# Optimization experiments

Measured on AMD Instinct MI355X. Metric: run time of the kernel, lower is better.

The kernel has to match this reference:

```python
import jax, jax.numpy as jnp
import numpy as np

NEG_INF = jnp.float32(-1e30)
EPS = 1e-7  # keras.backend.ctc_batch_cost epsilon


def ctc_batch_cost(y_true, y_pred):
    """Faithful CTC loss (keras ctc_batch_cost semantics): y_pred are
    probabilities [B,T,C], blank = C-1, full input/label lengths.
    Returns per-example negative log likelihood [B,1]."""
    B, T, C = y_pred.shape
    L = y_true.shape[1]
    S = 2 * L + 1  # extended label length (blanks interleaved)
    blank = C - 1

    log_probs = jnp.log(y_pred + EPS)  # [B,T,C]

    # Extended label sequence: blank, l0, blank, l1, ..., blank  -> [B,S]
    ext = jnp.full((B, S), blank, dtype=y_true.dtype)
    ext = ext.at[:, 1::2].set(y_true)

    # Skip transition allowed at s if ext[s] != blank and ext[s] != ext[s-2]
    skip = jnp.concatenate(
        [jnp.zeros((B, 2), dtype=bool),
         (ext[:, 2:] != blank) & (ext[:, 2:] != ext[:, :-2])], axis=1)  # [B,S]

    # Gather log-probs of extended labels per timestep: [T,B,S]
    lp_ext = jnp.take_along_axis(log_probs, ext[:, None, :], axis=2)  # [B,T,S]
    lp_ext = jnp.transpose(lp_ext, (1, 0, 2))  # [T,B,S]

    # alpha init at t=0: only positions 0 (blank) and 1 (first label)
    alpha0 = jnp.full((B, S), NEG_INF, dtype=log_probs.dtype)
    alpha0 = alpha0.at[:, 0].set(lp_ext[0, :, 0])
    alpha0 = alpha0.at[:, 1].set(lp_ext[0, :, 1])

    pad1 = jnp.full((B, 1), NEG_INF, dtype=log_probs.dtype)
    pad2 = jnp.full((B, 2), NEG_INF, dtype=log_probs.dtype)

    def step(alpha, lp_t):
        a_stay = alpha
        a_prev = jnp.concatenate([pad1, alpha[:, :-1]], axis=1)
        a_skip = jnp.where(skip, jnp.concatenate([pad2, alpha[:, :-2]], axis=1), NEG_INF)
        m = jnp.maximum(jnp.maximum(a_stay, a_prev), a_skip)
        lse = m + jnp.log(jnp.exp(a_stay - m) + jnp.exp(a_prev - m) + jnp.exp(a_skip - m))
        return lse + lp_t, None

    alpha_T, _ = jax.lax.scan(step, alpha0, lp_ext[1:])  # [B,S]

    # log P = logsumexp over last blank and last label positions
    end = jnp.stack([alpha_T[:, S - 1], alpha_T[:, S - 2]], axis=1)  # [B,2]
    loglik = jax.nn.logsumexp(end, axis=1)  # [B]
    return -loglik[:, None]  # [B,1] like keras ctc_batch_cost


def setup_inputs() -> dict:
    key = jax.random.key(0)
    k1, k2 = jax.random.split(key)
    B, T, C, L = 512, 512, 128, 32
    y_true = jax.random.randint(k1, (B, L), 0, C - 1, dtype=jnp.int64 if jax.config.read('jax_enable_x64') else jnp.int32)
    y_pred = jax.random.uniform(k2, (B, T, C), dtype=jnp.float32)
    return {"y_true": y_true, "y_pred": y_pred}


def reference(y_true, y_pred):
    return ctc_batch_cost(y_true, y_pred)
```

## Files before the change

### kernel.cpp

```cpp
#include <hip/hip_runtime.h>


#define EPSF 1e-7f

constexpr int T_  = 512;
constexpr int C_  = 128;
constexpr int L_  = 32;
constexpr int NG  = 127;
constexpr int PFG = 4;
constexpr int NLD = 17;

__launch_bounds__(64)
__global__ void ctc_loss_kernel(const int* __restrict__ y_true,
                                const float* __restrict__ y_pred,
                                float* __restrict__ out) {
    const int b    = blockIdx.x;
    const int lane = threadIdx.x;

    const float* bb  = y_pred + (size_t)b * T_ * C_;
    const int*   lbl = y_true + b * L_;

    int   cls[7];
    float sg[7];
#pragma unroll
    for (int i = 0; i < 7; ++i) {
        const int v = lane - i;
        int   c = C_ - 1;
        float s = 0.f;
        if (v >= 1 && (v & 1)) {
            c = lbl[(v - 1) >> 1];
            if (v >= 3 && c != lbl[((v - 1) >> 1) - 1]) s = 1.f;
        }
        cls[i] = c;
        sg[i]  = s;
    }
    float msk[9];
#pragma unroll
    for (int i = 0; i < 9; ++i) msk[i] = (lane >= i) ? 1.f : 0.f;

    float a       = (lane < 2) ? (bb[cls[0]] + EPSF) : 0.f;
    float a64     = 0.f;
    int   e_total = 0;

    float Q[PFG][NLD];
    auto loadq = [&](float (&Qk)[NLD], const float* __restrict__ r) {
        Qk[0]  = r[cls[0]];          Qk[1]  = r[cls[1]];
        Qk[2]  = r[cls[2]];          Qk[3]  = r[cls[3]];
        Qk[4]  = r[cls[4]];          Qk[5]  = r[cls[5]];
        Qk[6]  = r[cls[6]];
        Qk[7]  = r[C_ + cls[0]];     Qk[8]  = r[C_ + cls[1]];
        Qk[9]  = r[C_ + cls[2]];     Qk[10] = r[C_ + cls[3]];
        Qk[11] = r[C_ + cls[4]];
        Qk[12] = r[2 * C_ + cls[0]]; Qk[13] = r[2 * C_ + cls[1]];
        Qk[14] = r[2 * C_ + cls[2]];
        Qk[15] = r[3 * C_ + cls[0]]; Qk[16] = r[3 * C_ + cls[1]];
    };
#pragma unroll
    for (int k = 0; k < PFG; ++k) loadq(Q[k], bb + (size_t)(1 + 4 * k) * C_);

    float smp[16];
    auto sample = [&]() {
#pragma unroll
        for (int i = 0; i < 16; ++i) smp[i] = __shfl(a, 4 * i + 3);
    };
    sample();

    auto group4 = [&](float (&Qk)[NLD]) {
        float A[9];
        A[0] = a;
#pragma unroll
        for (int i = 1; i <= 8; ++i) A[i] = __shfl_up(a, i) * msk[i];

        float B[7];
#pragma unroll
        for (int i = 0; i <= 6; ++i)
            B[i] = (A[i] + A[i + 1] + sg[i] * A[i + 2]) * (Qk[i] + EPSF);
        float Cc[5];
#pragma unroll
        for (int i = 0; i <= 4; ++i)
            Cc[i] = (B[i] + B[i + 1] + sg[i] * B[i + 2]) * (Qk[7 + i] + EPSF);
        float D[3];
#pragma unroll
        for (int i = 0; i <= 2; ++i)
            D[i] = (Cc[i] + Cc[i + 1] + sg[i] * Cc[i + 2]) * (Qk[12 + i] + EPSF);

        float z = a64;
        z = (z + A[0])  * (Qk[1]  + EPSF);
        z = (z + B[0])  * (Qk[8]  + EPSF);
        z = (z + Cc[0]) * (Qk[13] + EPSF);
        z = (z + D[0])  * (Qk[16] + EPSF);
        a64 = z;

        a = (D[0] + D[1] + sg[0] * D[2]) * (Qk[15] + EPSF);
    };

    auto apply_scale = [&]() {
        float t[8];
#pragma unroll
        for (int i = 0; i < 8; ++i) t[i] = fmaxf(smp[i], smp[i + 8]);
#pragma unroll
        for (int i = 0; i < 4; ++i) t[i] = fmaxf(t[i], t[i + 4]);
        float m = fmaxf(fmaxf(t[0], t[1]), fmaxf(t[2], t[3]));
        m = fmaxf(m, 1e-30f);
        const unsigned eb = __float_as_uint(m) >> 23;
        e_total += (int)eb - 127;
        const float inv = __uint_as_float((254u - eb) << 23);
        a *= inv;
        a64 *= inv;
    };

    for (int g0 = 0; g0 < 124; g0 += PFG) {
#pragma unroll
        for (int k = 0; k < PFG; ++k) {
            const int g = g0 + k;
            group4(Q[k]);
            apply_scale();
            sample();
            const int gn = g + PFG;
            if (gn < NG) loadq(Q[k], bb + (size_t)(1 + 4 * gn) * C_);
        }
    }

    float qo[3], qb[3];
#pragma unroll
    for (int r = 0; r < 3; ++r) {
        const float* rp = bb + (size_t)(509 + r) * C_;
        qo[r] = rp[cls[0]];
        qb[r] = rp[cls[1]];
    }

    group4(Q[0]); apply_scale(); sample();
    group4(Q[1]); apply_scale(); sample();
    group4(Q[2]); apply_scale();

#pragma unroll
    for (int r = 0; r < 3; ++r) {
        float prev = __shfl_up(a, 1) * msk[1];
        float sk   = __shfl_up(a, 2) * msk[2];
        const float anew = (a + prev + sg[0] * sk) * (qo[r] + EPSF);
        a64 = (a64 + a) * (qb[r] + EPSF);
        a = anew;
    }

    if (lane == 63) {
        out[b] = -(__logf(a + a64) + (float)e_total * 0.6931471805599453f);
    }
}

extern "C" void kernel_launch(void* const* d_in, const int* in_sizes, int n_in,
                              void* d_out, int out_size, void* d_ws, size_t ws_size,
                              hipStream_t stream) {
    const int*   y_true = (const int*)d_in[0];
    const float* y_pred = (const float*)d_in[1];
    float*       out    = (float*)d_out;

    const int B = out_size;
    ctc_loss_kernel<<<B, 64, 0, stream>>>(y_true, y_pred, out);
}
```

Measured before the change: 225.3 us.

## Split CTC recursion into concurrent forward and backward passes meeting mid-sequence

Result: no change. 226.5 us (+0.6%).

```diff
diff --git a/kernel.cpp b/kernel.cpp
--- a/kernel.cpp
+++ b/kernel.cpp
@@ -3,74 +3,103 @@
 
 #define EPSF 1e-7f
 
-constexpr int T_  = 512;
-constexpr int C_  = 128;
-constexpr int L_  = 32;
-constexpr int NG  = 127;
-constexpr int PFG = 4;
-constexpr int NLD = 17;
+constexpr int T_ = 512;
+constexpr int C_ = 128;
+constexpr int L_ = 32;
+constexpr int NF = 17;
+constexpr int NB = 28;
 
 __launch_bounds__(64)
 __global__ void ctc_loss_kernel(const int* __restrict__ y_true,
                                 const float* __restrict__ y_pred,
                                 float* __restrict__ out) {
-    const int b    = blockIdx.x;
+    const int bidx = blockIdx.x;
     const int lane = threadIdx.x;
 
-    const float* bb  = y_pred + (size_t)b * T_ * C_;
-    const int*   lbl = y_true + b * L_;
-
-    int   cls[7];
+    const float* bb  = y_pred + (size_t)bidx * T_ * C_;
+    const int*   lbl = y_true + bidx * L_;
+
+    int   cf[7];
     float sg[7];
+    float msk[9];
 #pragma unroll
     for (int i = 0; i < 7; ++i) {
         const int v = lane - i;
-        int   c = C_ - 1;
-        float s = 0.f;
+        int c = C_ - 1; float s = 0.f;
         if (v >= 1 && (v & 1)) {
             c = lbl[(v - 1) >> 1];
             if (v >= 3 && c != lbl[((v - 1) >> 1) - 1]) s = 1.f;
         }
-        cls[i] = c;
-        sg[i]  = s;
-    }
-    float msk[9];
+        cf[i] = c * 4; sg[i] = s;
+    }
 #pragma unroll
     for (int i = 0; i < 9; ++i) msk[i] = (lane >= i) ? 1.f : 0.f;
 
-    float a       = (lane < 2) ? (bb[cls[0]] + EPSF) : 0.f;
-    float a64     = 0.f;
-    int   e_total = 0;
-
-    float Q[PFG][NLD];
-    auto loadq = [&](float (&Qk)[NLD], const float* __restrict__ r) {
-        Qk[0]  = r[cls[0]];          Qk[1]  = r[cls[1]];
-        Qk[2]  = r[cls[2]];          Qk[3]  = r[cls[3]];
-        Qk[4]  = r[cls[4]];          Qk[5]  = r[cls[5]];
-        Qk[6]  = r[cls[6]];
-        Qk[7]  = r[C_ + cls[0]];     Qk[8]  = r[C_ + cls[1]];
-        Qk[9]  = r[C_ + cls[2]];     Qk[10] = r[C_ + cls[3]];
-        Qk[11] = r[C_ + cls[4]];
-        Qk[12] = r[2 * C_ + cls[0]]; Qk[13] = r[2 * C_ + cls[1]];
-        Qk[14] = r[2 * C_ + cls[2]];
-        Qk[15] = r[3 * C_ + cls[0]]; Qk[16] = r[3 * C_ + cls[1]];
-    };
-#pragma unroll
-    for (int k = 0; k < PFG; ++k) loadq(Q[k], bb + (size_t)(1 + 4 * k) * C_);
-
-    float smp[16];
-    auto sample = [&]() {
-#pragma unroll
-        for (int i = 0; i < 16; ++i) smp[i] = __shfl(a, 4 * i + 3);
-    };
-    sample();
-
-    auto group4 = [&](float (&Qk)[NLD]) {
+    int   cb[9];
+    float gd[7];
+    float mdn[9];
+#pragma unroll
+    for (int i = 0; i < 9; ++i) {
+        const int u = lane + 1 + i;
+        int c = C_ - 1;
+        if (u <= 64 && (u & 1)) c = lbl[(u - 1) >> 1];
+        cb[i] = c * 4;
+        mdn[i] = (lane + i <= 63) ? 1.f : 0.f;
+    }
+#pragma unroll
+    for (int i = 0; i < 7; ++i) {
+        const int v = lane + i + 3;
+        float g = 0.f;
+        if (v <= 64 && (v & 1) && lbl[(v - 1) >> 1] != lbl[((v - 1) >> 1) - 1]) g = 1.f;
+        gd[i] = g;
+    }
+
+    auto gat = [](const float* r, int boff) -> float {
+        return *(const float*)((const char*)r + boff);
+    };
+
+    float a   = (lane < 2) ? (gat(bb, cf[0]) + EPSF) : 0.f;
+    float a64 = 0.f;
+    float b   = (lane >= 62) ? 1.f : 0.f;
+    float b0  = 0.f;
+    int ef = 0, eb = 0;
+
+    float Qf[3][NF];
+    float Qb[3][NB];
+
+    auto loadqf = [&](float (&Qk)[NF], const float* r) {
+        Qk[0]  = gat(r, cf[0]);          Qk[1]  = gat(r, cf[1]);
+        Qk[2]  = gat(r, cf[2]);          Qk[3]  = gat(r, cf[3]);
+        Qk[4]  = gat(r, cf[4]);          Qk[5]  = gat(r, cf[5]);
+        Qk[6]  = gat(r, cf[6]);
+        Qk[7]  = gat(r + C_, cf[0]);     Qk[8]  = gat(r + C_, cf[1]);
+        Qk[9]  = gat(r + C_, cf[2]);     Qk[10] = gat(r + C_, cf[3]);
+        Qk[11] = gat(r + C_, cf[4]);
+        Qk[12] = gat(r + 2*C_, cf[0]);   Qk[13] = gat(r + 2*C_, cf[1]);
+        Qk[14] = gat(r + 2*C_, cf[2]);
+        Qk[15] = gat(r + 3*C_, cf[0]);   Qk[16] = gat(r + 3*C_, cf[1]);
+    };
+    auto loadqb = [&](float (&Qk)[NB], const float* r3) {
+        const float* r2 = r3 - C_;
+        const float* r1 = r3 - 2*C_;
+        const float* r0 = r3 - 3*C_;
+#pragma unroll
+        for (int i = 0; i < 9; ++i) Qk[i]      = gat(r3, cb[i]);
+#pragma unroll
+        for (int i = 0; i < 7; ++i) Qk[9 + i]  = gat(r2, cb[i]);
+#pragma unroll
+        for (int i = 0; i < 5; ++i) Qk[16 + i] = gat(r1, cb[i]);
+#pragma unroll
+        for (int i = 0; i < 3; ++i) Qk[21 + i] = gat(r0, cb[i]);
+        Qk[24] = r3[C_ - 1]; Qk[25] = r2[C_ - 1];
+        Qk[26] = r1[C_ - 1]; Qk[27] = r0[C_ - 1];
+    };
+
+    auto fgroup4 = [&](float (&Qk)[NF]) {
         float A[9];
         A[0] = a;
 #pragma unroll
         for (int i = 1; i <= 8; ++i) A[i] = __shfl_up(a, i) * msk[i];
-
         float B[7];
 #pragma unroll
         for (int i = 0; i <= 6; ++i)
@@ -83,67 +112,143 @@
 #pragma unroll
         for (int i = 0; i <= 2; ++i)
             D[i] = (Cc[i] + Cc[i + 1] + sg[i] * Cc[i + 2]) * (Qk[12 + i] + EPSF);
-
         float z = a64;
         z = (z + A[0])  * (Qk[1]  + EPSF);
         z = (z + B[0])  * (Qk[8]  + EPSF);
         z = (z + Cc[0]) * (Qk[13] + EPSF);
         z = (z + D[0])  * (Qk[16] + EPSF);
         a64 = z;
-
         a = (D[0] + D[1] + sg[0] * D[2]) * (Qk[15] + EPSF);
     };
 
-    auto apply_scale = [&]() {
+    auto bgroup4 = [&](float (&Qk)[NB]) {
+        float BA[9];
+        BA[0] = b;
+#pragma unroll
+        for (int i = 1; i <= 8; ++i) BA[i] = __shfl_down(b, i) * mdn[i];
+        float G[9];
+#pragma unroll
+        for (int i = 0; i <= 8; ++i) G[i] = BA[i] * (Qk[i] + EPSF);
+        float X[7];
+#pragma unroll
+        for (int i = 0; i <= 6; ++i) X[i] = G[i] + G[i + 1] + gd[i] * G[i + 2];
+        float G2[7];
+#pragma unroll
+        for (int i = 0; i <= 6; ++i) G2[i] = X[i] * (Qk[9 + i] + EPSF);
+        float X2[5];
+#pragma unroll
+        for (int i = 0; i <= 4; ++i) X2[i] = G2[i] + G2[i + 1] + gd[i] * G2[i + 2];
+        float G3[5];
+#pragma unroll
+        for (int i = 0; i <= 4; ++i) G3[i] = X2[i] * (Qk[16 + i] + EPSF);
+        float X3[3];
+#pragma unroll
+        for (int i = 0; i <= 2; ++i) X3[i] = G3[i] + G3[i + 1] + gd[i] * G3[i + 2];
+        float G4[3];
+#pragma unroll
+        for (int i = 0; i <= 2; ++i) G4[i] = X3[i] * (Qk[21 + i] + EPSF);
+        float z = b0;
+        z = (Qk[24] + EPSF) * z + G[0];
+        z = (Qk[25] + EPSF) * z + G2[0];
+        z = (Qk[26] + EPSF) * z + G3[0];
+        z = (Qk[27] + EPSF) * z + G4[0];
+        b0 = z;
+        b = G4[0] + G4[1] + gd[0] * G4[2];
+    };
+
+    float smpF[16], smpB[16];
+    auto sampleF = [&]() {
+#pragma unroll
+        for (int i = 0; i < 16; ++i) smpF[i] = __shfl(a, 4 * i + 3);
+    };
+    auto sampleB = [&]() {
+#pragma unroll
+        for (int i = 0; i < 16; ++i) smpB[i] = __shfl(b, 4 * i + 3);
+    };
+    auto apply = [&](const float* s, float& x, float& y, int& e) {
         float t[8];
 #pragma unroll
-        for (int i = 0; i < 8; ++i) t[i] = fmaxf(smp[i], smp[i + 8]);
+        for (int i = 0; i < 8; ++i) t[i] = fmaxf(s[i], s[i + 8]);
 #pragma unroll
         for (int i = 0; i < 4; ++i) t[i] = fmaxf(t[i], t[i + 4]);
         float m = fmaxf(fmaxf(t[0], t[1]), fmaxf(t[2], t[3]));
-        m = fmaxf(m, 1e-30f);
-        const unsigned eb = __float_as_uint(m) >> 23;
-        e_total += (int)eb - 127;
-        const float inv = __uint_as_float((254u - eb) << 23);
-        a *= inv;
-        a64 *= inv;
-    };
-
-    for (int g0 = 0; g0 < 124; g0 += PFG) {
-#pragma unroll
-        for (int k = 0; k < PFG; ++k) {
-            const int g = g0 + k;
-            group4(Q[k]);
-            apply_scale();
-            sample();
-            const int gn = g + PFG;
-            if (gn < NG) loadq(Q[k], bb + (size_t)(1 + 4 * gn) * C_);
+        m = fmaxf(m, 9.094947e-13f);
+        int be = (int)(__float_as_uint(m) >> 23);
+        be = (be < 67) ? 67 : ((be > 187) ? 187 : be);
+        e += be - 127;
+        const float inv = __uint_as_float((unsigned)(254 - be) << 23);
+        x *= inv; y *= inv;
+    };
+
+#pragma unroll
+    for (int k = 0; k < 3; ++k) {
+        loadqf(Qf[k], bb + (size_t)(1 + 4 * k) * C_);
+        loadqb(Qb[k], bb + (size_t)(511 - 4 * k) * C_);
+    }
+    sampleF(); sampleB();
+
+    for (int i0 = 0; i0 < 63; i0 += 3) {
+#pragma unroll
+        for (int k = 0; k < 3; ++k) {
+            const int t = i0 + k;
+            fgroup4(Qf[k]);
+            bgroup4(Qb[k]);
+            if ((t & 1) == 0) { apply(smpF, a, a64, ef); sampleF(); }
+            else              { apply(smpB, b, b0, eb); sampleB(); }
+            const int gf = (t + 3 <= 63) ? (t + 3) : 63;
+            const int gb = (t + 3 <= 62) ? (t + 3) : 62;
+            loadqf(Qf[k], bb + (size_t)(1 + 4 * gf) * C_);
+            loadqb(Qb[k], bb + (size_t)(511 - 4 * gb) * C_);
         }
     }
 
-    float qo[3], qb[3];
+    float qs[12];
 #pragma unroll
     for (int r = 0; r < 3; ++r) {
-        const float* rp = bb + (size_t)(509 + r) * C_;
-        qo[r] = rp[cls[0]];
-        qb[r] = rp[cls[1]];
-    }
-
-    group4(Q[0]); apply_scale(); sample();
-    group4(Q[1]); apply_scale(); sample();
-    group4(Q[2]); apply_scale();
+        const float* row = bb + (size_t)(259 - r) * C_;
+        qs[4 * r + 0] = gat(row, cb[0]);
+        qs[4 * r + 1] = gat(row, cb[1]);
+        qs[4 * r + 2] = gat(row, cb[2]);
+        qs[4 * r + 3] = row[C_ - 1];
+    }
+
+    fgroup4(Qf[0]);
+    apply(smpF, a, a64, ef);
 
 #pragma unroll
     for (int r = 0; r < 3; ++r) {
-        float prev = __shfl_up(a, 1) * msk[1];
-        float sk   = __shfl_up(a, 2) * msk[2];
-        const float anew = (a + prev + sg[0] * sk) * (qo[r] + EPSF);
-        a64 = (a64 + a) * (qb[r] + EPSF);
-        a = anew;
-    }
-
-    if (lane == 63) {
-        out[b] = -(__logf(a + a64) + (float)e_total * 0.6931471805599453f);
+        const float g0  = b * (qs[4 * r + 0] + EPSF);
+        const float ba1 = __shfl_down(b, 1) * mdn[1];
+        const float ba2 = __shfl_down(b, 2) * mdn[2];
+        const float g1  = ba1 * (qs[4 * r + 1] + EPSF);
+        const float g2  = ba2 * (qs[4 * r + 2] + EPSF);
+        b0 = (qs[4 * r + 3] + EPSF) * b0 + g0;
+        b  = g0 + g1 + gd[0] * g2;
+    }
+
+    const float NEGB = -1e30f;
+    auto lg = [&](float v) -> float { return (v > 0.f) ? __logf(v) : NEGB; };
+    const float la   = lg(a);
+    const float lb   = lg(b);
+    const float ladn = __shfl_down(la, 1);
+    float t1 = (lane <= 62) ? (ladn + lb) : NEGB;
+    float t2 = NEGB;
+    if (lane == 0)  t2 = la + lg(b0);
+    if (lane == 63) t2 = lg(a64) + lb;
+
+    float wmax = fmaxf(t1, t2);
+#pragma unroll
+    for (int off = 1; off < 64; off <<= 1) wmax = fmaxf(wmax, __shfl_xor(wmax, off));
+
+    const float e1 = (t1 > -1e29f) ? __expf(t1 - wmax) : 0.f;
+    const float e2 = (t2 > -1e29f) ? __expf(t2 - wmax) : 0.f;
+    float p = e1 + e2;
+#pragma unroll
+    for (int off = 1; off < 64; off <<= 1) p += __shfl_xor(p, off);
+
+    if (lane == 0) {
+        const float ll = wmax + __logf(p) + (float)(ef + eb) * 0.6931471805599453f;
+        out[bidx] = -ll;
     }
 }
 
```
